# Kernel tuning notes

Hardware: AMD Instinct MI355X
Metric: run time of the kernel (lower is better)

## Reference

```python
import jax, jax.numpy as jnp
import numpy as np

B, S, D, H, PF = 2, 2048, 1024, 16, 4096
HD = D // H
EPS = 1e-5


def _rope_tables(seq_len, dim, theta=10000.0):
    freqs = 1.0 / (theta ** (np.arange(0, dim, 2)[: dim // 2].astype(np.float32) / dim))
    ang = np.outer(np.arange(seq_len, dtype=np.float32), freqs)  # [S, D/2]
    return jnp.asarray(np.cos(ang)), jnp.asarray(np.sin(ang))


def setup_inputs() -> dict:
    key = jax.random.key(0)
    ks = jax.random.split(key, 16)
    s = 0.02
    inp = {
        "src": jax.random.normal(ks[0], (B, S, D), dtype=jnp.float32),
        "Wq": jax.random.normal(ks[1], (D, D), dtype=jnp.float32) * s,
        "bq": jnp.zeros((D,), jnp.float32),
        "Wk": jax.random.normal(ks[2], (D, D), dtype=jnp.float32) * s,
        "bk": jnp.zeros((D,), jnp.float32),
        "Wv": jax.random.normal(ks[3], (D, D), dtype=jnp.float32) * s,
        "bv": jnp.zeros((D,), jnp.float32),
        "Wo": jax.random.normal(ks[4], (D, D), dtype=jnp.float32) * s,
        "bo": jnp.zeros((D,), jnp.float32),
        "ln1_g": jnp.ones((D,), jnp.float32),
        "ln1_b": jnp.zeros((D,), jnp.float32),
        "W1": jax.random.normal(ks[5], (D, PF), dtype=jnp.float32) * s,
        "b1": jnp.zeros((PF,), jnp.float32),
        "W2": jax.random.normal(ks[6], (PF, D), dtype=jnp.float32) * s,
        "b2": jnp.zeros((D,), jnp.float32),
        "ln2_g": jnp.ones((D,), jnp.float32),
        "ln2_b": jnp.zeros((D,), jnp.float32),
    }
    cos, sin = _rope_tables(S, D)
    inp["rope_cos"] = cos
    inp["rope_sin"] = sin
    return inp


def _apply_rope(x, cos, sin):
    # x: [B, S, D]; rotate adjacent channel pairs as complex numbers (Meta LLaMA style)
    xp = x.reshape(x.shape[0], x.shape[1], -1, 2)
    a, b = xp[..., 0], xp[..., 1]
    c = cos[None, : x.shape[1]]
    s = sin[None, : x.shape[1]]
    out = jnp.stack([a * c - b * s, a * s + b * c], axis=-1)
    return out.reshape(x.shape)


def _layer_norm(x, g, b):
    mu = x.mean(-1, keepdims=True)
    var = ((x - mu) ** 2).mean(-1, keepdims=True)
    return (x - mu) * jax.lax.rsqrt(var + EPS) * g + b


def reference(src, Wq, bq, Wk, bk, Wv, bv, Wo, bo, ln1_g, ln1_b,
              W1, b1, W2, b2, ln2_g, ln2_b, rope_cos, rope_sin):
    bsz, seq, _ = src.shape
    Q = src @ Wq + bq
    K = src @ Wk + bk
    V = src @ Wv + bv
    Q = _apply_rope(Q, rope_cos, rope_sin)
    K = _apply_rope(K, rope_cos, rope_sin)
    # split heads: [B, H, S, HD]
    Q = Q.reshape(bsz, seq, H, HD).transpose(0, 2, 1, 3)
    K = K.reshape(bsz, seq, H, HD).transpose(0, 2, 1, 3)
    V = V.reshape(bsz, seq, H, HD).transpose(0, 2, 1, 3)
    scale = 1.0 / jnp.sqrt(jnp.float32(HD))
    energy = jnp.einsum("bhqd,bhkd->bhqk", Q, K) * scale
    attn = jax.nn.softmax(energy, axis=-1)
    x = jnp.einsum("bhqk,bhkd->bhqd", attn, V)
    x = x.transpose(0, 2, 1, 3).reshape(bsz, seq, D)
    attn_out = x @ Wo + bo
    # residual + LayerNorm
    h = _layer_norm(src + attn_out, ln1_g, ln1_b)
    # positionwise feedforward
    ff = jax.nn.relu(h @ W1 + b1) @ W2 + b2
    return _layer_norm(h + ff, ln2_g, ln2_b)
```

## Files before the change

kernel.cpp:

```cpp
#include <hip/hip_runtime.h>

#define SEQ 2048
#define DIM 1024
#define NH 16
#define HDIM 64
#define PFF 4096
#define NROWS 4096
#define BATCH 2
#define NQKV 3072

typedef unsigned short u16;
typedef unsigned int u32;
typedef __attribute__((ext_vector_type(8))) short short8;
typedef __attribute__((ext_vector_type(4))) float f32x4;
typedef __attribute__((ext_vector_type(16))) float f32x16;

__device__ inline float b2f(u16 u){ return __uint_as_float(((u32)u)<<16); }
__device__ inline u16 f2b(float f){
  u32 u = __float_as_uint(f);
  u32 r = u + 0x7FFFu + ((u>>16)&1u);
  return (u16)(r>>16);
}
__device__ __forceinline__ float fexp2(float x){
  float r; asm("v_exp_f32 %0, %1" : "=v"(r) : "v"(x)); return r;
}

#define AS1C(p) ((const __attribute__((address_space(1))) unsigned int*)(p))
#define AS3P(p) ((__attribute__((address_space(3))) unsigned int*)(p))

__global__ void k_cast_bf16(const float* __restrict__ in, u16* __restrict__ out, int n4){
  int i = blockIdx.x*256 + threadIdx.x;
  if (i >= n4) return;
  float4 v = ((const float4*)in)[i];
  ushort4 o;
  o.x = f2b(v.x); o.y = f2b(v.y); o.z = f2b(v.z); o.w = f2b(v.w);
  ((ushort4*)out)[i] = o;
}

__global__ __launch_bounds__(256) void k_transpose_cast(const float* __restrict__ in,
                                                        u16* __restrict__ out, int R, int C){
  __shared__ float tile[32][33];
  int tx = threadIdx.x & 31, ty = threadIdx.x >> 5;
  int c0 = blockIdx.x*32, r0 = blockIdx.y*32;
  #pragma unroll
  for (int i=0;i<4;++i)
    tile[ty+i*8][tx] = in[(size_t)(r0+ty+i*8)*C + c0 + tx];
  __syncthreads();
  #pragma unroll
  for (int i=0;i<4;++i)
    out[(size_t)(c0+ty+i*8)*R + r0 + tx] = f2b(tile[tx][ty+i*8]);
}

__global__ __launch_bounds__(256) void k_transpose_cast4(
    const float* __restrict__ w0, const float* __restrict__ w1,
    const float* __restrict__ w2, const float* __restrict__ w3,
    u16* __restrict__ o012, u16* __restrict__ o3){
  __shared__ float tile[32][33];
  const int z = blockIdx.z;
  const float* in = z==0 ? w0 : (z==1 ? w1 : (z==2 ? w2 : w3));
  u16* out = (z<3) ? (o012 + (size_t)z*DIM*DIM) : o3;
  int tx = threadIdx.x & 31, ty = threadIdx.x >> 5;
  int c0 = blockIdx.x*32, r0 = blockIdx.y*32;
  #pragma unroll
  for (int i=0;i<4;++i)
    tile[ty+i*8][tx] = in[(size_t)(r0+ty+i*8)*DIM + c0 + tx];
  __syncthreads();
  #pragma unroll
  for (int i=0;i<4;++i)
    out[(size_t)(c0+ty+i*8)*DIM + r0 + tx] = f2b(tile[tx][ty+i*8]);
}

__global__ __launch_bounds__(256) void k_transpose_v(const u16* __restrict__ QKV, u16* __restrict__ VT){
  __shared__ u16 tile[32][34];
  int tx = threadIdx.x & 31, ty = threadIdx.x >> 5;
  int d0 = blockIdx.x*32, r0 = blockIdx.y*32;
  #pragma unroll
  for (int i=0;i<4;++i)
    tile[ty+i*8][tx] = QKV[(size_t)(r0+ty+i*8)*NQKV + 2048 + d0 + tx];
  __syncthreads();
  #pragma unroll
  for (int i=0;i<4;++i)
    VT[(size_t)(d0+ty+i*8)*NROWS + r0 + tx] = tile[tx][ty+i*8];
}

__global__ void k_pack3(const float* __restrict__ a, const float* __restrict__ b,
                        const float* __restrict__ c, float* __restrict__ o){
  int i = blockIdx.x*256 + threadIdx.x;
  if (i >= NQKV) return;
  o[i] = i < 1024 ? a[i] : (i < 2048 ? b[i-1024] : c[i-2048]);
}

template<bool RELU, bool BF16OUT, int SPLIT>
__global__ __launch_bounds__(512, 2) void k_gemm256(
    const u16* __restrict__ A, const u16* __restrict__ Bt,
    const float* __restrict__ bias, void* __restrict__ Cp,
    int M, int N, int Kc, int lda, int ldb){
  extern __shared__ char lds[];
  const int tid = threadIdx.x;
  const int lane = tid & 63, wid = tid >> 6;
  const int quad = lane >> 4, l15 = lane & 15;
  const int wm = wid >> 2, wn = wid & 3;
  const int ro = (l15*4 + quad)*16;
  const int srow = lane >> 2;
  const int sk   = (lane & 3)*8;
  const int nwg = gridDim.x * gridDim.y;
  int lid = blockIdx.y * gridDim.x + blockIdx.x;
  lid = (lid & 7) * (nwg >> 3) + (lid >> 3);
  const int bx = lid % gridDim.x, by = lid / gridDim.x;
  const int rowBase = by*256, colBase = bx*256;
  const u16* Az = A  + (size_t)blockIdx.z * Kc;
  const u16* Bz = Bt + (size_t)blockIdx.z * Kc;

  f32x4 acc[8][4] = {};

  auto stage2 = [&](int buf, int k0, int i){
    int idx = i*8 + wid;
    int rs = idx >> 1, ks = idx & 1;
    const u16* ga = Az + (size_t)(rowBase + rs*16 + srow)*lda + k0 + ks*32 + sk;
    __builtin_amdgcn_global_load_lds(AS1C(ga), AS3P(lds + buf*65536 + idx*1024), 16, 0, 0);
    const u16* gb = Bz + (size_t)(colBase + rs*16 + srow)*ldb + k0 + ks*32 + sk;
    __builtin_amdgcn_global_load_lds(AS1C(gb), AS3P(lds + buf*65536 + 32768 + idx*1024), 16, 0, 0);
  };

  #pragma unroll
  for (int i=0;i<4;++i) stage2(0, 0, i);
  __syncthreads();

  const int NT = Kc >> 6;
  #pragma unroll 1
  for (int t=0; t<NT; ++t){
    const int buf = t & 1;
    const bool pf = (t+1 < NT);
    const int k0n = (t+1)*64;
    char* Ab = lds + buf*65536;
    char* Bb = Ab + 32768;
    short8 a0[4][2], a1[4][2], b0[2][2], b1[2][2];

    #pragma unroll
    for (int mf=0; mf<4; ++mf)
      #pragma unroll
      for (int kk=0; kk<2; ++kk)
        a0[mf][kk] = *(const short8*)(Ab + ((wm*8+mf)*2+kk)*1024 + ro);
    #pragma unroll
    for (int nf=0; nf<2; ++nf)
      #pragma unroll
      for (int kk=0; kk<2; ++kk)
        b0[nf][kk] = *(const short8*)(Bb + ((wn*4+nf)*2+kk)*1024 + ro);
    if (pf){ stage2(buf^1, k0n, 0); stage2(buf^1, k0n, 1); }
    __builtin_amdgcn_s_barrier();
    __builtin_amdgcn_s_setprio(1);
    #pragma unroll
    for (int mf=0; mf<4; ++mf)
      #pragma unroll
      for (int nf=0; nf<2; ++nf)
        #pragma unroll
        for (int kk=0; kk<2; ++kk)
          acc[mf][nf] = __builtin_amdgcn_mfma_f32_16x16x32_bf16(a0[mf][kk], b0[nf][kk], acc[mf][nf], 0,0,0);
    __builtin_amdgcn_s_setprio(0);
    __builtin_amdgcn_s_barrier();

    #pragma unroll
    for (int nf=0; nf<2; ++nf)
      #pragma unroll
      for (int kk=0; kk<2; ++kk)
        b1[nf][kk] = *(const short8*)(Bb + ((wn*4+2+nf)*2+kk)*1024 + ro);
    if (pf){ stage2(buf^1, k0n, 2); stage2(buf^1, k0n, 3); }
    __builtin_amdgcn_s_barrier();
    __builtin_amdgcn_s_setprio(1);
    #pragma unroll
    for (int mf=0; mf<4; ++mf)
      #pragma unroll
      for (int nf=0; nf<2; ++nf)
        #pragma unroll
        for (int kk=0; kk<2; ++kk)
          acc[mf][2+nf] = __builtin_amdgcn_mfma_f32_16x16x32_bf16(a0[mf][kk], b1[nf][kk], acc[mf][2+nf], 0,0,0);
    __builtin_amdgcn_s_setprio(0);
    __builtin_amdgcn_s_barrier();

    #pragma unroll
    for (int mf=0; mf<4; ++mf)
      #pragma unroll
      for (int kk=0; kk<2; ++kk)
        a1[mf][kk] = *(const short8*)(Ab + ((wm*8+4+mf)*2+kk)*1024 + ro);
    __builtin_amdgcn_s_barrier();
    __builtin_amdgcn_s_setprio(1);
    #pragma unroll
    for (int mf=0; mf<4; ++mf)
      #pragma unroll
      for (int nf=0; nf<2; ++nf)
        #pragma unroll
        for (int kk=0; kk<2; ++kk)
          acc[4+mf][2+nf] = __builtin_amdgcn_mfma_f32_16x16x32_bf16(a1[mf][kk], b1[nf][kk], acc[4+mf][2+nf], 0,0,0);
    __builtin_amdgcn_s_setprio(0);
    __builtin_amdgcn_s_barrier();

    if (pf) asm volatile("s_waitcnt vmcnt(0)" ::: "memory");
    __builtin_amdgcn_s_barrier();
    __builtin_amdgcn_s_setprio(1);
    #pragma unroll
    for (int mf=0; mf<4; ++mf)
      #pragma unroll
      for (int nf=0; nf<2; ++nf)
        #pragma unroll
        for (int kk=0; kk<2; ++kk)
          acc[4+mf][nf] = __builtin_amdgcn_mfma_f32_16x16x32_bf16(a1[mf][kk], b0[nf][kk], acc[4+mf][nf], 0,0,0);
    __builtin_amdgcn_s_setprio(0);
    __builtin_amdgcn_s_barrier();
  }

  u16* Cb = (u16*)Cp + (SPLIT > 1 ? (size_t)blockIdx.z * M * N : 0);
  float* Cf = (float*)Cp + (SPLIT > 1 ? (size_t)blockIdx.z * M * N : 0);
  #pragma unroll
  for (int mf=0; mf<8; ++mf){
    #pragma unroll
    for (int nf=0; nf<4; ++nf){
      int col = colBase + wn*64 + nf*16 + l15;
      float bv = (SPLIT == 1 || blockIdx.z == 0) ? bias[col] : 0.f;
      #pragma unroll
      for (int j=0; j<4; ++j){
        int row = rowBase + wm*128 + mf*16 + quad*4 + j;
        float v = acc[mf][nf][j] + bv;
        if (RELU) v = fmaxf(v, 0.f);
        if (BF16OUT) Cb[(size_t)row*N + col] = f2b(v);
        else         Cf[(size_t)row*N + col] = v;
      }
    }
  }
}

__global__ void k_rope(u16* __restrict__ QKV,
                       const float* __restrict__ cosT, const float* __restrict__ sinT){
  int idx = blockIdx.x*256 + threadIdx.x;
  int row = idx >> 9, p = idx & 511;
  int s = row & (SEQ-1);
  float c = cosT[s*512 + p], sn = sinT[s*512 + p];
  u16* qp = QKV + (size_t)row*NQKV + 2*p;
  u16* kp = qp + 1024;
  ushort2 q = *(ushort2*)qp;
  ushort2 k = *(ushort2*)kp;
  float qx = b2f(q.x), qy = b2f(q.y), kx = b2f(k.x), ky = b2f(k.y);
  const float scale = 0.125f * 1.44269504f;
  ushort2 qo, ko;
  qo.x = f2b((qx*c - qy*sn)*scale);
  qo.y = f2b((qx*sn + qy*c)*scale);
  ko.x = f2b(kx*c - ky*sn);
  ko.y = f2b(kx*sn + ky*c);
  *(ushort2*)qp = qo;
  *(ushort2*)kp = ko;
}

__global__ __launch_bounds__(256) void k_attn(
    const u16* __restrict__ QKV, const u16* __restrict__ VT, u16* __restrict__ Xo){
  const int qt = blockIdx.x, h = blockIdx.y, b = blockIdx.z;
  const int tid = threadIdx.x, lane = tid & 63, wid = tid >> 6;
  const int l31 = lane & 31, hi = lane >> 5;
  __shared__ __align__(16) char lds[32768];
  const int srow = lane >> 3, scol = lane & 7;

  short8 qf[4];
  {
    const u16* qrow = QKV + (size_t)(b*SEQ + qt*128 + wid*32 + l31)*NQKV + h*HDIM;
    #pragma unroll
    for (int dk=0; dk<4; ++dk)
      qf[dk] = *(const short8*)(qrow + dk*16 + 8*hi);
  }
  float s_run = 0.f;
  f32x16 oacc[2] = {};
  const size_t krow0 = (size_t)(b*SEQ);

  auto do_stage = [&](int buf, int kt){
    char* kdst = lds + buf*16384;
    char* vdst = kdst + 8192;
    #pragma unroll
    for (int i=0;i<2;++i){
      int wch = wid*2 + i;
      int row = wch*8 + srow;
      int c = scol ^ (row & 7);
      const u16* gk = QKV + (krow0 + kt*64 + row)*NQKV + 1024 + h*HDIM + c*8;
      __builtin_amdgcn_global_load_lds(AS1C(gk), AS3P(kdst + wch*1024), 16, 0, 0);
      const u16* gv = VT + (size_t)(h*HDIM + row)*NROWS + b*SEQ + kt*64 + c*8;
      __builtin_amdgcn_global_load_lds(AS1C(gv), AS3P(vdst + wch*1024), 16, 0, 0);
    }
  };

  auto do_tile = [&](int buf){
    char* kb = lds + buf*16384;
    char* vb = kb + 8192;
    f32x16 pacc[2] = {};
    __builtin_amdgcn_s_setprio(1);
    #pragma unroll
    for (int kbk=0;kbk<2;++kbk){
      #pragma unroll
      for (int dk=0;dk<4;++dk){
        int row = kbk*32 + l31;
        short8 kf = *(const short8*)(kb + ((row*128 + dk*32 + 16*hi) ^ ((row&7)<<4)));
        pacc[kbk] = __builtin_amdgcn_mfma_f32_32x32x16_bf16(kf, qf[dk], pacc[kbk], 0,0,0);
      }
    }
    __builtin_amdgcn_s_setprio(0);
    float psum = 0.f;
    short8 pa[4];
    #pragma unroll
    for (int kbk=0;kbk<2;++kbk){
      #pragma unroll
      for (int s=0;s<2;++s){
        float e0 = fexp2(pacc[kbk][8*s+0]);
        float e1 = fexp2(pacc[kbk][8*s+1]);
        float e2 = fexp2(pacc[kbk][8*s+2]);
        float e3 = fexp2(pacc[kbk][8*s+3]);
        float e4 = fexp2(pacc[kbk][8*s+4]);
        float e5 = fexp2(pacc[kbk][8*s+5]);
        float e6 = fexp2(pacc[kbk][8*s+6]);
        float e7 = fexp2(pacc[kbk][8*s+7]);
        psum += (e0+e1)+(e2+e3)+((e4+e5)+(e6+e7));
        u32 X0, X1, Y0, Y1;
        asm("v_cvt_pk_bf16_f32 %0, %1, %2" : "=v"(X0) : "v"(e0), "v"(e1));
        asm("v_cvt_pk_bf16_f32 %0, %1, %2" : "=v"(X1) : "v"(e2), "v"(e3));
        asm("v_cvt_pk_bf16_f32 %0, %1, %2" : "=v"(Y0) : "v"(e4), "v"(e5));
        asm("v_cvt_pk_bf16_f32 %0, %1, %2" : "=v"(Y1) : "v"(e6), "v"(e7));
        asm volatile("v_permlane32_swap_b32 %0, %1" : "+v"(X0), "+v"(Y0));
        asm volatile("v_permlane32_swap_b32 %0, %1" : "+v"(X1), "+v"(Y1));
        union { u32 w[4]; short8 s8; } pu;
        pu.w[0] = X0; pu.w[1] = X1; pu.w[2] = Y0; pu.w[3] = Y1;
        pa[2*kbk+s] = pu.s8;
      }
    }
    psum += __shfl_xor(psum, 32);
    s_run += psum;
    __builtin_amdgcn_s_setprio(1);
    #pragma unroll
    for (int db=0;db<2;++db){
      #pragma unroll
      for (int ks=0;ks<4;++ks){
        int row = db*32 + l31;
        short8 vf = *(const short8*)(vb + ((row*128 + ks*32 + 16*hi) ^ ((row&7)<<4)));
        oacc[db] = __builtin_amdgcn_mfma_f32_32x32x16_bf16(pa[ks], vf, oacc[db], 0,0,0);
      }
    }
    __builtin_amdgcn_s_setprio(0);
  };

  do_stage(0, 0);
  __syncthreads();
  const int NT = SEQ/64;
  #pragma unroll 1
  for (int kt=0; kt<NT; kt+=2){
    do_stage(1, kt+1);
    do_tile(0);
    __syncthreads();
    if (kt+2 < NT) do_stage(0, kt+2);
    do_tile(1);
    __syncthreads();
  }
  #pragma unroll
  for (int r=0;r<16;++r){
    int crow = (r&3) + 8*(r>>2) + 4*hi;
    float sq = __shfl(s_run, crow);
    float rs = __builtin_amdgcn_rcpf(sq);
    int grow = b*SEQ + qt*128 + wid*32 + crow;
    Xo[(size_t)grow*DIM + h*HDIM + l31]      = f2b(oacc[0][r] * rs);
    Xo[(size_t)grow*DIM + h*HDIM + 32 + l31] = f2b(oacc[1][r] * rs);
  }
}

template<int PARTS, bool WF32, bool WBF, bool RESBF>
__global__ __launch_bounds__(256) void k_lnp(
    const void* __restrict__ a, const u16* __restrict__ p,
    const float* __restrict__ g, const float* __restrict__ be,
    float* __restrict__ outf, u16* __restrict__ outb){
  const int row = blockIdx.x, tid = threadIdx.x;
  __shared__ float red[8];
  float x0, x1, x2, x3;
  if (RESBF){
    ushort4 av = ((const ushort4*)((const u16*)a + (size_t)row*DIM))[tid];
    x0 = b2f(av.x); x1 = b2f(av.y); x2 = b2f(av.z); x3 = b2f(av.w);
  } else {
    float4 av = ((const float4*)((const float*)a + (size_t)row*DIM))[tid];
    x0 = av.x; x1 = av.y; x2 = av.z; x3 = av.w;
  }
  #pragma unroll
  for (int z=0; z<PARTS; ++z){
    ushort4 pv = ((const ushort4*)(p + (size_t)z*NROWS*DIM + (size_t)row*DIM))[tid];
    x0 += b2f(pv.x); x1 += b2f(pv.y); x2 += b2f(pv.z); x3 += b2f(pv.w);
  }
  float s = x0+x1+x2+x3;
  #pragma unroll
  for (int o=32;o>=1;o>>=1) s += __shfl_down(s, o);
  if ((tid&63)==0) red[tid>>6] = s;
  __syncthreads();
  float mean = (red[0]+red[1]+red[2]+red[3]) * (1.0f/DIM);
  float d0=x0-mean, d1=x1-mean, d2=x2-mean, d3=x3-mean;
  float vs = d0*d0+d1*d1+d2*d2+d3*d3;
  #pragma unroll
  for (int o=32;o>=1;o>>=1) vs += __shfl_down(vs, o);
  if ((tid&63)==0) red[4+(tid>>6)] = vs;
  __syncthreads();
  float var = (red[4]+red[5]+red[6]+red[7]) * (1.0f/DIM);
  float rs = rsqrtf(var + 1e-5f);
  float4 gv = ((const float4*)g)[tid];
  float4 bev = ((const float4*)be)[tid];
  float4 y;
  y.x = d0*rs*gv.x + bev.x;
  y.y = d1*rs*gv.y + bev.y;
  y.z = d2*rs*gv.z + bev.z;
  y.w = d3*rs*gv.w + bev.w;
  if (WF32)
    ((float4*)(outf + (size_t)row*DIM))[tid] = y;
  if (WBF){
    ushort4 o4; o4.x=f2b(y.x); o4.y=f2b(y.y); o4.z=f2b(y.z); o4.w=f2b(y.w);
    ((ushort4*)(outb + (size_t)row*DIM))[tid] = o4;
  }
}

extern "C" void kernel_launch(void* const* d_in, const int* in_sizes, int n_in,
                              void* d_out, int out_size, void* d_ws, size_t ws_size,
                              hipStream_t stream){
  (void)in_sizes; (void)n_in; (void)out_size; (void)ws_size;
  const float* src  = (const float*)d_in[0];
  const float* Wq   = (const float*)d_in[1];
  const float* bq   = (const float*)d_in[2];
  const float* Wk   = (const float*)d_in[3];
  const float* bk   = (const float*)d_in[4];
  const float* Wv   = (const float*)d_in[5];
  const float* bv   = (const float*)d_in[6];
  const float* Wo   = (const float*)d_in[7];
  const float* bo   = (const float*)d_in[8];
  const float* ln1g = (const float*)d_in[9];
  const float* ln1b = (const float*)d_in[10];
  const float* W1   = (const float*)d_in[11];
  const float* b1   = (const float*)d_in[12];
  const float* W2   = (const float*)d_in[13];
  const float* b2   = (const float*)d_in[14];
  const float* ln2g = (const float*)d_in[15];
  const float* ln2b = (const float*)d_in[16];
  const float* rc   = (const float*)d_in[17];
  const float* rsn  = (const float*)d_in[18];

  char* ws = (char*)d_ws;
  const size_t MB = (size_t)1<<20;
  u16* Xbf   = (u16*)(ws);
  u16* QKV   = (u16*)(ws + 8*MB);
  u16* VTb   = (u16*)(ws + 32*MB);
  u16* aob   = (u16*)(ws + 8*MB);
  u16* ff2b  = (u16*)(ws + 8*MB);
  u16* xat   = (u16*)(ws + 40*MB);
  u16* hbf   = (u16*)(ws + 48*MB);
  u16* WqkvT = (u16*)(ws + 56*MB);
  u16* WoT   = (u16*)(ws + 62*MB);
  u16* W1T   = (u16*)(ws + 64*MB);
  u16* W2T   = (u16*)(ws + 72*MB);
  u16* ff1   = (u16*)(ws + 80*MB);
  float* bqkv= (float*)(ws + 128*MB);

  hipFuncSetAttribute((const void*)&k_gemm256<false,true,1>,
                      hipFuncAttributeMaxDynamicSharedMemorySize, 131072);
  hipFuncSetAttribute((const void*)&k_gemm256<true,true,1>,
                      hipFuncAttributeMaxDynamicSharedMemorySize, 131072);
  hipFuncSetAttribute((const void*)&k_gemm256<false,true,4>,
                      hipFuncAttributeMaxDynamicSharedMemorySize, 131072);

  dim3 blk(256);
  k_cast_bf16<<<dim3(NROWS*DIM/1024), blk, 0, stream>>>(src, Xbf, NROWS*DIM/4);
  k_transpose_cast4<<<dim3(DIM/32, DIM/32, 4), blk, 0, stream>>>(Wq, Wk, Wv, Wo, WqkvT, WoT);
  k_transpose_cast<<<dim3(PFF/32, DIM/32), blk, 0, stream>>>(W1, W1T, DIM, PFF);
  k_transpose_cast<<<dim3(DIM/32, PFF/32), blk, 0, stream>>>(W2, W2T, PFF, DIM);
  k_pack3<<<dim3(12), blk, 0, stream>>>(bq, bk, bv, bqkv);

  k_gemm256<false,true,1><<<dim3(NQKV/256, NROWS/256), dim3(512), 131072, stream>>>(
      Xbf, WqkvT, bqkv, QKV, NROWS, NQKV, DIM, DIM, DIM);
  k_rope<<<dim3(NROWS*512/256), blk, 0, stream>>>(QKV, rc, rsn);
  k_transpose_v<<<dim3(DIM/32, NROWS/32), blk, 0, stream>>>(QKV, VTb);
  k_attn<<<dim3(SEQ/128, NH, BATCH), blk, 0, stream>>>(QKV, VTb, xat);
  k_gemm256<false,true,4><<<dim3(DIM/256, NROWS/256, 4), dim3(512), 131072, stream>>>(
      xat, WoT, bo, aob, NROWS, DIM, 256, DIM, DIM);
  k_lnp<4,false,true,false><<<dim3(NROWS), blk, 0, stream>>>(
      src, aob, ln1g, ln1b, nullptr, hbf);
  k_gemm256<true,true,1><<<dim3(PFF/256, NROWS/256), dim3(512), 131072, stream>>>(
      hbf, W1T, b1, ff1, NROWS, PFF, DIM, DIM, DIM);
  k_gemm256<false,true,4><<<dim3(DIM/256, NROWS/256, 4), dim3(512), 131072, stream>>>(
      ff1, W2T, b2, ff2b, NROWS, DIM, 1024, PFF, PFF);
  k_lnp<4,true,false,true><<<dim3(NROWS), blk, 0, stream>>>(
      hbf, ff2b, ln2g, ln2b, (float*)d_out, nullptr);
}
```

Measured before the change: 244.1 us.

## Fuse RoPE into QKV GEMM epilogue and double attention KV tile size

Applies rotary embedding and the Q softmax scale inside the QKV GEMM epilogue, using a lane shuffle to fetch the paired channel, which removes the separate k_rope kernel and its read-modify-write pass over Q and K. The attention kernel now stages 128 keys per tile instead of 64, using 64KB of LDS, with a new swizzle layout for V. This halves loop iterations and barriers but raises LDS use and register pressure, which may reduce occupancy.

```diff
diff --git a/kernel.cpp b/kernel.cpp
--- a/kernel.cpp
+++ b/kernel.cpp
@@ -90,11 +90,12 @@
   o[i] = i < 1024 ? a[i] : (i < 2048 ? b[i-1024] : c[i-2048]);
 }
 
-template<bool RELU, bool BF16OUT, int SPLIT>
+template<bool RELU, bool BF16OUT, int SPLIT, bool ROPE>
 __global__ __launch_bounds__(512, 2) void k_gemm256(
     const u16* __restrict__ A, const u16* __restrict__ Bt,
     const float* __restrict__ bias, void* __restrict__ Cp,
-    int M, int N, int Kc, int lda, int ldb){
+    int M, int N, int Kc, int lda, int ldb,
+    const float* __restrict__ rcT, const float* __restrict__ rsT){
   extern __shared__ char lds[];
   const int tid = threadIdx.x;
   const int lane = tid & 63, wid = tid >> 6;
@@ -220,33 +221,24 @@
       for (int j=0; j<4; ++j){
         int row = rowBase + wm*128 + mf*16 + quad*4 + j;
         float v = acc[mf][nf][j] + bv;
+        if (ROPE){
+          if (col < 2048){
+            int sp = row & (SEQ-1);
+            int p  = (col & 1023) >> 1;
+            float c  = rcT[sp*512 + p];
+            float sn = rsT[sp*512 + p];
+            float vp = __shfl_xor(v, 1);
+            float rv = (l15 & 1) ? (vp*sn + v*c) : (v*c - vp*sn);
+            if (col < 1024) rv *= 0.18033688f;
+            v = rv;
+          }
+        }
         if (RELU) v = fmaxf(v, 0.f);
         if (BF16OUT) Cb[(size_t)row*N + col] = f2b(v);
         else         Cf[(size_t)row*N + col] = v;
       }
     }
   }
-}
-
-__global__ void k_rope(u16* __restrict__ QKV,
-                       const float* __restrict__ cosT, const float* __restrict__ sinT){
-  int idx = blockIdx.x*256 + threadIdx.x;
-  int row = idx >> 9, p = idx & 511;
-  int s = row & (SEQ-1);
-  float c = cosT[s*512 + p], sn = sinT[s*512 + p];
-  u16* qp = QKV + (size_t)row*NQKV + 2*p;
-  u16* kp = qp + 1024;
-  ushort2 q = *(ushort2*)qp;
-  ushort2 k = *(ushort2*)kp;
-  float qx = b2f(q.x), qy = b2f(q.y), kx = b2f(k.x), ky = b2f(k.y);
-  const float scale = 0.125f * 1.44269504f;
-  ushort2 qo, ko;
-  qo.x = f2b((qx*c - qy*sn)*scale);
-  qo.y = f2b((qx*sn + qy*c)*scale);
-  ko.x = f2b(kx*c - ky*sn);
-  ko.y = f2b(kx*sn + ky*c);
-  *(ushort2*)qp = qo;
-  *(ushort2*)kp = ko;
 }
 
 __global__ __launch_bounds__(256) void k_attn(
@@ -254,8 +246,9 @@
   const int qt = blockIdx.x, h = blockIdx.y, b = blockIdx.z;
   const int tid = threadIdx.x, lane = tid & 63, wid = tid >> 6;
   const int l31 = lane & 31, hi = lane >> 5;
-  __shared__ __align__(16) char lds[32768];
+  __shared__ __align__(16) char lds[65536];
   const int srow = lane >> 3, scol = lane & 7;
+  const int vrow4 = lane >> 4, vslot = lane & 15;
 
   short8 qf[4];
   {
@@ -269,39 +262,45 @@
   const size_t krow0 = (size_t)(b*SEQ);
 
   auto do_stage = [&](int buf, int kt){
-    char* kdst = lds + buf*16384;
-    char* vdst = kdst + 8192;
-    #pragma unroll
-    for (int i=0;i<2;++i){
-      int wch = wid*2 + i;
+    char* kdst = lds + buf*32768;
+    char* vdst = kdst + 16384;
+    #pragma unroll
+    for (int i=0;i<4;++i){
+      int wch = wid*4 + i;
       int row = wch*8 + srow;
       int c = scol ^ (row & 7);
-      const u16* gk = QKV + (krow0 + kt*64 + row)*NQKV + 1024 + h*HDIM + c*8;
+      const u16* gk = QKV + (krow0 + kt*128 + row)*NQKV + 1024 + h*HDIM + c*8;
       __builtin_amdgcn_global_load_lds(AS1C(gk), AS3P(kdst + wch*1024), 16, 0, 0);
-      const u16* gv = VT + (size_t)(h*HDIM + row)*NROWS + b*SEQ + kt*64 + c*8;
+    }
+    #pragma unroll
+    for (int i=0;i<4;++i){
+      int wch = wid*4 + i;
+      int row = wch*4 + vrow4;
+      int c = vslot ^ (row & 7);
+      const u16* gv = VT + (size_t)(h*HDIM + row)*NROWS + b*SEQ + kt*128 + c*8;
       __builtin_amdgcn_global_load_lds(AS1C(gv), AS3P(vdst + wch*1024), 16, 0, 0);
     }
   };
 
   auto do_tile = [&](int buf){
-    char* kb = lds + buf*16384;
-    char* vb = kb + 8192;
-    f32x16 pacc[2] = {};
-    __builtin_amdgcn_s_setprio(1);
-    #pragma unroll
-    for (int kbk=0;kbk<2;++kbk){
+    char* kb = lds + buf*32768;
+    char* vb = kb + 16384;
+    f32x16 pacc[4] = {};
+    __builtin_amdgcn_s_setprio(1);
+    #pragma unroll
+    for (int kbk=0;kbk<4;++kbk){
       #pragma unroll
       for (int dk=0;dk<4;++dk){
         int row = kbk*32 + l31;
-        short8 kf = *(const short8*)(kb + ((row*128 + dk*32 + 16*hi) ^ ((row&7)<<4)));
+        short8 kf = *(const short8*)(kb + row*128 + ((dk*32 + 16*hi) ^ ((row&7)<<4)));
         pacc[kbk] = __builtin_amdgcn_mfma_f32_32x32x16_bf16(kf, qf[dk], pacc[kbk], 0,0,0);
       }
     }
     __builtin_amdgcn_s_setprio(0);
     float psum = 0.f;
-    short8 pa[4];
-    #pragma unroll
-    for (int kbk=0;kbk<2;++kbk){
+    short8 pa[8];
+    #pragma unroll
+    for (int kbk=0;kbk<4;++kbk){
       #pragma unroll
       for (int s=0;s<2;++s){
         float e0 = fexp2(pacc[kbk][8*s+0]);
@@ -331,9 +330,9 @@
     #pragma unroll
     for (int db=0;db<2;++db){
       #pragma unroll
-      for (int ks=0;ks<4;++ks){
+      for (int ks=0;ks<8;++ks){
         int row = db*32 + l31;
-        short8 vf = *(const short8*)(vb + ((row*128 + ks*32 + 16*hi) ^ ((row&7)<<4)));
+        short8 vf = *(const short8*)(vb + row*256 + (((ks*2+hi)*16) ^ ((row&7)<<4)));
         oacc[db] = __builtin_amdgcn_mfma_f32_32x32x16_bf16(pa[ks], vf, oacc[db], 0,0,0);
       }
     }
@@ -342,7 +341,7 @@
 
   do_stage(0, 0);
   __syncthreads();
-  const int NT = SEQ/64;
+  const int NT = SEQ/128;
   #pragma unroll 1
   for (int kt=0; kt<NT; kt+=2){
     do_stage(1, kt+1);
@@ -452,11 +451,11 @@
   u16* ff1   = (u16*)(ws + 80*MB);
   float* bqkv= (float*)(ws + 128*MB);
 
-  hipFuncSetAttribute((const void*)&k_gemm256<false,true,1>,
+  hipFuncSetAttribute((const void*)&k_gemm256<false,true,1,true>,
                       hipFuncAttributeMaxDynamicSharedMemorySize, 131072);
-  hipFuncSetAttribute((const void*)&k_gemm256<true,true,1>,
+  hipFuncSetAttribute((const void*)&k_gemm256<true,true,1,false>,
                       hipFuncAttributeMaxDynamicSharedMemorySize, 131072);
-  hipFuncSetAttribute((const void*)&k_gemm256<false,true,4>,
+  hipFuncSetAttribute((const void*)&k_gemm256<false,true,4,false>,
                       hipFuncAttributeMaxDynamicSharedMemorySize, 131072);
 
   dim3 blk(256);
@@ -466,19 +465,18 @@
   k_transpose_cast<<<dim3(DIM/32, PFF/32), blk, 0, stream>>>(W2, W2T, PFF, DIM);
   k_pack3<<<dim3(12), blk, 0, stream>>>(bq, bk, bv, bqkv);
 
-  k_gemm256<false,true,1><<<dim3(NQKV/256, NROWS/256), dim3(512), 131072, stream>>>(
-      Xbf, WqkvT, bqkv, QKV, NROWS, NQKV, DIM, DIM, DIM);
-  k_rope<<<dim3(NROWS*512/256), blk, 0, stream>>>(QKV, rc, rsn);
+  k_gemm256<false,true,1,true><<<dim3(NQKV/256, NROWS/256), dim3(512), 131072, stream>>>(
+      Xbf, WqkvT, bqkv, QKV, NROWS, NQKV, DIM, DIM, DIM, rc, rsn);
   k_transpose_v<<<dim3(DIM/32, NROWS/32), blk, 0, stream>>>(QKV, VTb);
   k_attn<<<dim3(SEQ/128, NH, BATCH), blk, 0, stream>>>(QKV, VTb, xat);
-  k_gemm256<false,true,4><<<dim3(DIM/256, NROWS/256, 4), dim3(512), 131072, stream>>>(
-      xat, WoT, bo, aob, NROWS, DIM, 256, DIM, DIM);
+  k_gemm256<false,true,4,false><<<dim3(DIM/256, NROWS/256, 4), dim3(512), 131072, stream>>>(
+      xat, WoT, bo, aob, NROWS, DIM, 256, DIM, DIM, nullptr, nullptr);
   k_lnp<4,false,true,false><<<dim3(NROWS), blk, 0, stream>>>(
       src, aob, ln1g, ln1b, nullptr, hbf);
-  k_gemm256<true,true,1><<<dim3(PFF/256, NROWS/256), dim3(512), 131072, stream>>>(
-      hbf, W1T, b1, ff1, NROWS, PFF, DIM, DIM, DIM);
-  k_gemm256<false,true,4><<<dim3(DIM/256, NROWS/256, 4), dim3(512), 131072, stream>>>(
-      ff1, W2T, b2, ff2b, NROWS, DIM, 1024, PFF, PFF);
+  k_gemm256<true,true,1,false><<<dim3(PFF/256, NROWS/256), dim3(512), 131072, stream>>>(
+      hbf, W1T, b1, ff1, NROWS, PFF, DIM, DIM, DIM, nullptr, nullptr);
+  k_gemm256<false,true,4,false><<<dim3(DIM/256, NROWS/256, 4), dim3(512), 131072, stream>>>(
+      ff1, W2T, b2, ff2b, NROWS, DIM, 1024, PFF, PFF, nullptr, nullptr);
   k_lnp<4,true,false,true><<<dim3(NROWS), blk, 0, stream>>>(
       hbf, ff2b, ln2g, ln2b, (float*)d_out, nullptr);
 }
```

Result: slower. 272.4 us (+11.6%).
